# Performance work log

Hardware: AMD Instinct MI355X
Metric: run time of the kernel (lower is better)

Reference implementation:

```python
import jax, jax.numpy as jnp
import numpy as np


def _rconv(x, w, b):
    # reflection-pad 1 then 3x3 valid conv (same spatial size), NCHW/OIHW
    xp = jnp.pad(x, ((0, 0), (0, 0), (1, 1), (1, 1)), mode='reflect')
    y = jax.lax.conv_general_dilated(
        xp, w, window_strides=(1, 1), padding='VALID',
        dimension_numbers=('NCHW', 'OIHW', 'NCHW'))
    return y + b[None, :, None, None]


def setup_inputs() -> dict:
    key = jax.random.key(0)
    ks = jax.random.split(key, 12)
    B, C, H, W = 4, 256, 64, 64
    IC = 128  # inter_channels
    s = lambda fan_in: 1.0 / np.sqrt(fan_in)
    return {
        'query_feat': jax.random.normal(ks[0], (B, C, H, W), jnp.float32),
        'key_feat': jax.random.normal(ks[1], (B, C, H, W), jnp.float32),
        # 1x1 conv projections (stored as [out, in])
        'w_theta': jax.random.normal(ks[2], (IC, C), jnp.float32) * s(C),
        'b_theta': jnp.zeros((IC,), jnp.float32),
        'w_phi': jax.random.normal(ks[3], (IC, C), jnp.float32) * s(C),
        'b_phi': jnp.zeros((IC,), jnp.float32),
        # post-correlation block: conv(1->32), residual(32), conv(32->1)
        'w_in': jax.random.normal(ks[4], (32, 1, 3, 3), jnp.float32) * s(9),
        'b_in': jnp.zeros((32,), jnp.float32),
        'w_r1': jax.random.normal(ks[5], (32, 32, 3, 3), jnp.float32) * s(32 * 9),
        'b_r1': jnp.zeros((32,), jnp.float32),
        'w_r2': jax.random.normal(ks[6], (32, 32, 3, 3), jnp.float32) * s(32 * 9),
        'b_r2': jnp.zeros((32,), jnp.float32),
        'w_out': jax.random.normal(ks[7], (1, 32, 3, 3), jnp.float32) * s(32 * 9),
        'b_out': jnp.zeros((1,), jnp.float32),
    }


def reference(query_feat, key_feat, w_theta, b_theta, w_phi, b_phi,
              w_in, b_in, w_r1, b_r1, w_r2, b_r2, w_out, b_out):
    B, C, H, W = query_feat.shape
    N = H * W
    # 1x1 conv projections, flattened to sequences
    theta = jnp.einsum('oc,bchw->bohw', w_theta, query_feat) + b_theta[None, :, None, None]
    phi = jnp.einsum('oc,bchw->bohw', w_phi, key_feat) + b_phi[None, :, None, None]
    theta = theta.reshape(B, -1, N).transpose(0, 2, 1)  # [B, N, IC]
    phi = phi.reshape(B, -1, N)                          # [B, IC, N]
    # correlation matrix [B, N, N] then max over key positions
    f = jnp.matmul(theta, phi)
    sim = jnp.max(f, axis=-1).reshape(B, 1, H, W)
    # post-correlation conv refinement
    h = _rconv(sim, w_in, b_in)                      # 1 -> 32
    r = jax.nn.relu(_rconv(h, w_r1, b_r1))           # residual block
    r = _rconv(r, w_r2, b_r2)
    h = h + r
    out = _rconv(h, w_out, b_out)                    # 32 -> 1
    return out
```

## Files before the change

### kernel.cpp

```cpp
#include <hip/hip_runtime.h>

#define B_ 4
#define C_ 256
#define HH 64
#define WW 64
#define N_ 4096
#define IC_ 128
#define JC_ 8

typedef __attribute__((ext_vector_type(8))) short bf16x8;
typedef __attribute__((ext_vector_type(4))) float f32x4;

__device__ __forceinline__ short f2bf(float f) {
    unsigned u = __builtin_bit_cast(unsigned, f);
    unsigned r = (u + 0x7FFFu + ((u >> 16) & 1u)) >> 16;
    return (short)r;
}

__device__ __forceinline__ int refl(int v) {
    return v < 0 ? -v : (v > 63 ? 126 - v : v);
}

__global__ __launch_bounds__(256) void k_project(
    const float* __restrict__ qf, const float* __restrict__ kf,
    const float* __restrict__ wq, const float* __restrict__ wk,
    const float* __restrict__ bq, const float* __restrict__ bk,
    short* __restrict__ outq, short* __restrict__ outk) {
    int z = blockIdx.z;
    const float* x = z ? kf : qf;
    const float* wf = z ? wk : wq;
    const float* bias = z ? bk : bq;
    short* outT = z ? outk : outq;

    int b = blockIdx.y;
    int n0 = blockIdx.x * 64;
    int t = threadIdx.x;
    int lane = t & 63, wv = t >> 6;
    int l15 = lane & 15, q4 = lane >> 4;
    const float* xb = x + (size_t)b * C_ * N_;

    __shared__ float xs[2][32][68];

    f32x4 acc[8];
#pragma unroll
    for (int cf = 0; cf < 8; cf++) acc[cf] = (f32x4){0.f, 0.f, 0.f, 0.f};

    {
        int i0 = t, i1 = t + 256;
        int r0 = i0 >> 4, c0 = i0 & 15;
        int r1 = i1 >> 4, c1 = i1 & 15;
        *(f32x4*)(&xs[0][r0][c0 * 4]) = *(const f32x4*)(xb + (size_t)r0 * N_ + n0 + c0 * 4);
        *(f32x4*)(&xs[0][r1][c1 * 4]) = *(const f32x4*)(xb + (size_t)r1 * N_ + n0 + c1 * 4);
    }

    for (int ks = 0; ks < 8; ks++) {
        __syncthreads();
        int buf = ks & 1;
        if (ks < 7) {
            int cb = (ks + 1) * 32;
            int i0 = t, i1 = t + 256;
            int r0 = i0 >> 4, c0 = i0 & 15;
            int r1 = i1 >> 4, c1 = i1 & 15;
            *(f32x4*)(&xs[buf ^ 1][r0][c0 * 4]) =
                *(const f32x4*)(xb + (size_t)(cb + r0) * N_ + n0 + c0 * 4);
            *(f32x4*)(&xs[buf ^ 1][r1][c1 * 4]) =
                *(const f32x4*)(xb + (size_t)(cb + r1) * N_ + n0 + c1 * 4);
        }
        int cbase = ks * 32 + q4 * 8;
        bf16x8 a;
#pragma unroll
        for (int j = 0; j < 8; j++) a[j] = f2bf(xs[buf][q4 * 8 + j][wv * 16 + l15]);
#pragma unroll
        for (int cf = 0; cf < 8; cf++) {
            const float* wp = wf + (size_t)(cf * 16 + l15) * C_ + cbase;
            f32x4 wa = *(const f32x4*)wp;
            f32x4 wb = *(const f32x4*)(wp + 4);
            bf16x8 bfr;
            bfr[0] = f2bf(wa[0]); bfr[1] = f2bf(wa[1]);
            bfr[2] = f2bf(wa[2]); bfr[3] = f2bf(wa[3]);
            bfr[4] = f2bf(wb[0]); bfr[5] = f2bf(wb[1]);
            bfr[6] = f2bf(wb[2]); bfr[7] = f2bf(wb[3]);
            acc[cf] = __builtin_amdgcn_mfma_f32_16x16x32_bf16(a, bfr, acc[cf], 0, 0, 0);
        }
    }
#pragma unroll
    for (int cf = 0; cf < 8; cf++) {
        int ic = cf * 16 + l15;
        float bv = bias[ic];
#pragma unroll
        for (int r = 0; r < 4; r++) {
            int n = n0 + wv * 16 + q4 * 4 + r;
            outT[((size_t)b * N_ + n) * IC_ + ic] = f2bf(acc[cf][r] + bv);
        }
    }
}

__global__ __launch_bounds__(256, 4) void k_corr(const short* __restrict__ thetaT,
                                                 const short* __restrict__ phiT,
                                                 float* __restrict__ simp) {
    __shared__ short ph[2][64][136];

    int b = blockIdx.z, jc = blockIdx.y;
    int i0 = blockIdx.x * 128;
    int t = threadIdx.x;
    int lane = t & 63, w = t >> 6;
    int l15 = lane & 15, q4 = lane >> 4;

    const short* thb = thetaT + ((size_t)b * N_ + i0 + w * 32) * IC_;
    const short* phb = phiT + ((size_t)b * N_ + jc * (N_ / JC_)) * IC_;

    bf16x8 afr[2][4];
#pragma unroll
    for (int rf = 0; rf < 2; rf++)
#pragma unroll
        for (int ks = 0; ks < 4; ks++)
            afr[rf][ks] = *(const bf16x8*)(thb + (size_t)(rf * 16 + l15) * IC_ + ks * 32 + q4 * 8);

    int srow = t >> 4, sc8 = t & 15;
#pragma unroll
    for (int k = 0; k < 4; k++)
        *(bf16x8*)(&ph[0][srow + k * 16][sc8 * 8]) =
            *(const bf16x8*)(phb + (size_t)(srow + k * 16) * IC_ + sc8 * 8);

    f32x4 rmax[2];
#pragma unroll
    for (int rf = 0; rf < 2; rf++) rmax[rf] = (f32x4){-3.0e38f, -3.0e38f, -3.0e38f, -3.0e38f};

    const int NT = (N_ / JC_) / 64;
    for (int it = 0; it < NT; it++) {
        int buf = it & 1;
        __syncthreads();
        if (it < NT - 1) {
            int j0 = (it + 1) * 64;
#pragma unroll
            for (int k = 0; k < 4; k++)
                *(bf16x8*)(&ph[buf ^ 1][srow + k * 16][sc8 * 8]) =
                    *(const bf16x8*)(phb + (size_t)(j0 + srow + k * 16) * IC_ + sc8 * 8);
        }
#pragma unroll
        for (int jf = 0; jf < 4; jf++) {
            bf16x8 bfr[4];
#pragma unroll
            for (int ks = 0; ks < 4; ks++)
                bfr[ks] = *(const bf16x8*)(&ph[buf][jf * 16 + l15][ks * 32 + q4 * 8]);
#pragma unroll
            for (int rf = 0; rf < 2; rf++) {
                f32x4 a2 = (f32x4){0.f, 0.f, 0.f, 0.f};
#pragma unroll
                for (int ks = 0; ks < 4; ks++)
                    a2 = __builtin_amdgcn_mfma_f32_16x16x32_bf16(afr[rf][ks], bfr[ks], a2, 0, 0, 0);
#pragma unroll
                for (int r = 0; r < 4; r++) rmax[rf][r] = fmaxf(rmax[rf][r], a2[r]);
            }
        }
    }

#pragma unroll
    for (int rf = 0; rf < 2; rf++) {
#pragma unroll
        for (int r = 0; r < 4; r++) {
            float v = rmax[rf][r];
            v = fmaxf(v, __shfl_xor(v, 1));
            v = fmaxf(v, __shfl_xor(v, 2));
            v = fmaxf(v, __shfl_xor(v, 4));
            v = fmaxf(v, __shfl_xor(v, 8));
            rmax[rf][r] = v;
        }
    }
    if (l15 == 0) {
        float* sp = simp + ((size_t)(b * JC_ + jc)) * N_ + i0 + w * 32;
#pragma unroll
        for (int rf = 0; rf < 2; rf++)
#pragma unroll
            for (int r = 0; r < 4; r++) sp[rf * 16 + q4 * 4 + r] = rmax[rf][r];
    }
}

__global__ __launch_bounds__(256) void k_conv_in(const float* __restrict__ simp,
                                                 const float* __restrict__ w,
                                                 const float* __restrict__ bias,
                                                 float* __restrict__ h) {
    int y = blockIdx.x, b = blockIdx.y;
    int t = threadIdx.x;
    int oc = t >> 3, x8 = t & 7;
    __shared__ float srow[3][66];
    const float* sb = simp + (size_t)b * JC_ * N_;
    if (t < 192) {
        int r = t >> 6, x = t & 63;
        int idx = refl(y - 1 + r) * 64 + x;
        float v = -3.0e38f;
#pragma unroll
        for (int jc = 0; jc < JC_; jc++) v = fmaxf(v, sb[jc * N_ + idx]);
        srow[r][x + 1] = v;
    }
    if (t < 3) {
        int gy = refl(y - 1 + t);
        float vl = -3.0e38f, vr = -3.0e38f;
#pragma unroll
        for (int jc = 0; jc < JC_; jc++) {
            vl = fmaxf(vl, sb[jc * N_ + gy * 64 + 1]);
            vr = fmaxf(vr, sb[jc * N_ + gy * 64 + 62]);
        }
        srow[t][0] = vl;
        srow[t][65] = vr;
    }
    __syncthreads();

    float wr[9];
#pragma unroll
    for (int k = 0; k < 9; k++) wr[k] = w[oc * 9 + k];
    float bv = bias[oc];
    float acc[8];
#pragma unroll
    for (int xi = 0; xi < 8; xi++) acc[xi] = bv;
#pragma unroll
    for (int ky = 0; ky < 3; ky++)
#pragma unroll
        for (int kx = 0; kx < 3; kx++) {
            float wv2 = wr[ky * 3 + kx];
#pragma unroll
            for (int xi = 0; xi < 8; xi++) acc[xi] += wv2 * srow[ky][x8 * 8 + xi + kx];
        }
    float* op = h + (((size_t)b * 32 + oc) * 64 + y) * 64 + x8 * 8;
#pragma unroll
    for (int xi = 0; xi < 8; xi++) op[xi] = acc[xi];
}

template <bool RELU, bool ADD>
__global__ __launch_bounds__(256) void k_conv_r(const float* __restrict__ in,
                                                const float* __restrict__ w,
                                                const float* __restrict__ bias,
                                                float* __restrict__ out,
                                                const float* __restrict__ add) {
    int y = blockIdx.x, b = blockIdx.z;
    int oc0 = blockIdx.y * 16;
    int t = threadIdx.x;
    __shared__ float tile[32][3][68];
    __shared__ float wlds[32 * 16 * 12];

#pragma unroll
    for (int k = 0; k < 18; k++) {
        int id = t + k * 256;
        int ocl = id / 288;
        int rem = id - ocl * 288;
        int ic = rem / 9;
        int tap = rem - ic * 9;
        wlds[(ic * 16 + ocl) * 12 + tap] = w[(size_t)(oc0 + ocl) * 288 + rem];
    }

#pragma unroll
    for (int r = 0; r < 3; r++) {
        int gy = refl(y - 1 + r);
#pragma unroll
        for (int i = 0; i < 2; i++) {
            int idx = t + i * 256;
            int ic = idx >> 4, c4 = idx & 15;
            f32x4 v = *(const f32x4*)(in + (((size_t)b * 32 + ic) * 64 + gy) * 64 + c4 * 4);
#pragma unroll
            for (int s = 0; s < 4; s++) tile[ic][r][c4 * 4 + s + 1] = v[s];
        }
    }
    if (t < 96) {
        int ic = t / 3, r = t - ic * 3;
        int gy = refl(y - 1 + r);
        const float* row = in + (((size_t)b * 32 + ic) * 64 + gy) * 64;
        tile[ic][r][0] = row[1];
        tile[ic][r][65] = row[62];
    }
    __syncthreads();

    int ocl = t >> 4, x4 = (t & 15) * 4;
    float bv = bias[oc0 + ocl];
    float acc[4];
#pragma unroll
    for (int xi = 0; xi < 4; xi++) acc[xi] = bv;

#pragma unroll 2
    for (int ic = 0; ic < 32; ic++) {
        const float* wr = &wlds[(ic * 16 + ocl) * 12];
        f32x4 W0 = *(const f32x4*)(wr);
        f32x4 W1 = *(const f32x4*)(wr + 4);
        f32x4 W2 = *(const f32x4*)(wr + 8);
        float w0 = W0[0], w1 = W0[1], w2 = W0[2], w3 = W0[3];
        float w4 = W1[0], w5 = W1[1], w6 = W1[2], w7 = W1[3];
        float w8 = W2[0];
        float xr[3][8];
#pragma unroll
        for (int r = 0; r < 3; r++) {
            const float* rowp = &tile[ic][r][x4];
            f32x4 A = *(const f32x4*)(rowp);
            f32x4 Bv = *(const f32x4*)(rowp + 4);
            xr[r][0] = A[0]; xr[r][1] = A[1]; xr[r][2] = A[2]; xr[r][3] = A[3];
            xr[r][4] = Bv[0]; xr[r][5] = Bv[1]; xr[r][6] = Bv[2]; xr[r][7] = Bv[3];
        }
#pragma unroll
        for (int xi = 0; xi < 4; xi++) {
            acc[xi] += w0 * xr[0][xi] + w1 * xr[0][xi + 1] + w2 * xr[0][xi + 2] +
                       w3 * xr[1][xi] + w4 * xr[1][xi + 1] + w5 * xr[1][xi + 2] +
                       w6 * xr[2][xi] + w7 * xr[2][xi + 1] + w8 * xr[2][xi + 2];
        }
    }
    size_t off = (((size_t)b * 32 + oc0 + ocl) * 64 + y) * 64 + x4;
#pragma unroll
    for (int xi = 0; xi < 4; xi++) {
        float v = acc[xi];
        if (RELU) v = fmaxf(v, 0.f);
        if (ADD) v += add[off + xi];
        out[off + xi] = v;
    }
}

__global__ __launch_bounds__(256) void k_conv_out(const float* __restrict__ hb,
                                                  const float* __restrict__ w,
                                                  const float* __restrict__ bias,
                                                  float* __restrict__ outp) {
    int y = blockIdx.x, b = blockIdx.y;
    int t = threadIdx.x;
    int x = t & 63, g = t >> 6;
    __shared__ float red[4][64];
    __shared__ float wl[288];
    for (int k = t; k < 288; k += 256) wl[k] = w[k];
    __syncthreads();
    float acc = 0.f;
#pragma unroll
    for (int i = 0; i < 8; i++) {
        int ic = g * 8 + i;
        const float* wp = wl + ic * 9;
#pragma unroll
        for (int ky = 0; ky < 3; ky++) {
            int gy = refl(y + ky - 1);
            const float* row = hb + (((size_t)b * 32 + ic) * 64 + gy) * 64;
#pragma unroll
            for (int kx = 0; kx < 3; kx++) {
                int gx = refl(x + kx - 1);
                acc += wp[ky * 3 + kx] * row[gx];
            }
        }
    }
    red[g][x] = acc;
    __syncthreads();
    if (t < 64) {
        outp[((size_t)b * 64 + y) * 64 + x] =
            bias[0] + red[0][t] + red[1][t] + red[2][t] + red[3][t];
    }
}

extern "C" void kernel_launch(void* const* d_in, const int* in_sizes, int n_in,
                              void* d_out, int out_size, void* d_ws, size_t ws_size,
                              hipStream_t stream) {
    const float* q = (const float*)d_in[0];
    const float* kf = (const float*)d_in[1];
    const float* w_theta = (const float*)d_in[2];
    const float* b_theta = (const float*)d_in[3];
    const float* w_phi = (const float*)d_in[4];
    const float* b_phi = (const float*)d_in[5];
    const float* w_in = (const float*)d_in[6];
    const float* b_in = (const float*)d_in[7];
    const float* w_r1 = (const float*)d_in[8];
    const float* b_r1 = (const float*)d_in[9];
    const float* w_r2 = (const float*)d_in[10];
    const float* b_r2 = (const float*)d_in[11];
    const float* w_out = (const float*)d_in[12];
    const float* b_out = (const float*)d_in[13];
    float* out = (float*)d_out;

    char* ws = (char*)d_ws;
    short* thetaT = (short*)(ws);
    short* phiT = (short*)(ws + 4194304);
    float* simp = (float*)(ws + 8519680);
    float* h = (float*)(ws);
    float* r = (float*)(ws + 2097152);

    k_project<<<dim3(64, 4, 2), 256, 0, stream>>>(q, kf, w_theta, w_phi, b_theta, b_phi,
                                                  thetaT, phiT);
    k_corr<<<dim3(32, JC_, 4), 256, 0, stream>>>(thetaT, phiT, simp);
    k_conv_in<<<dim3(64, 4), 256, 0, stream>>>(simp, w_in, b_in, h);
    k_conv_r<true, false><<<dim3(64, 2, 4), 256, 0, stream>>>(h, w_r1, b_r1, r, nullptr);
    k_conv_r<false, true><<<dim3(64, 2, 4), 256, 0, stream>>>(r, w_r2, b_r2, h, h);
    k_conv_out<<<dim3(64, 4), 256, 0, stream>>>(h, w_out, b_out, out);
}
```

Measured before the change: 187.2 us.

## Pre-convert projection weights to bf16 and retile projection over output channels

Adds a small kernel that converts the theta/phi weight matrices to bf16 once per call, so the projection kernel loads bf16x8 fragments directly instead of loading fp32 and converting inside the inner loop. The projection tile shrinks from 64 to 32 spatial positions, which doubles the grid. Each wave now covers 32 output channels across two row fragments, so every weight fragment is reused for two MFMAs, where before each wave did all 128 channels for 16 positions. This cuts redundant weight conversion and global weight traffic per block, at the cost of one extra kernel launch and more blocks that each reload their own input tile.

```diff
diff --git a/kernel.cpp b/kernel.cpp
--- a/kernel.cpp
+++ b/kernel.cpp
@@ -21,76 +21,78 @@
     return v < 0 ? -v : (v > 63 ? 126 - v : v);
 }
 
+__global__ __launch_bounds__(256) void k_cvt_w(const float* __restrict__ wt,
+                                               const float* __restrict__ wp,
+                                               short* __restrict__ wtb,
+                                               short* __restrict__ wpb) {
+    int i = blockIdx.x * 256 + threadIdx.x;
+    wtb[i] = f2bf(wt[i]);
+    wpb[i] = f2bf(wp[i]);
+}
+
 __global__ __launch_bounds__(256) void k_project(
     const float* __restrict__ qf, const float* __restrict__ kf,
-    const float* __restrict__ wq, const float* __restrict__ wk,
+    const short* __restrict__ wq, const short* __restrict__ wk,
     const float* __restrict__ bq, const float* __restrict__ bk,
     short* __restrict__ outq, short* __restrict__ outk) {
     int z = blockIdx.z;
     const float* x = z ? kf : qf;
-    const float* wf = z ? wk : wq;
+    const short* wbf = z ? wk : wq;
     const float* bias = z ? bk : bq;
     short* outT = z ? outk : outq;
 
     int b = blockIdx.y;
-    int n0 = blockIdx.x * 64;
+    int n0 = blockIdx.x * 32;
     int t = threadIdx.x;
     int lane = t & 63, wv = t >> 6;
     int l15 = lane & 15, q4 = lane >> 4;
     const float* xb = x + (size_t)b * C_ * N_;
 
-    __shared__ float xs[2][32][68];
-
-    f32x4 acc[8];
-#pragma unroll
-    for (int cf = 0; cf < 8; cf++) acc[cf] = (f32x4){0.f, 0.f, 0.f, 0.f};
-
-    {
-        int i0 = t, i1 = t + 256;
-        int r0 = i0 >> 4, c0 = i0 & 15;
-        int r1 = i1 >> 4, c1 = i1 & 15;
-        *(f32x4*)(&xs[0][r0][c0 * 4]) = *(const f32x4*)(xb + (size_t)r0 * N_ + n0 + c0 * 4);
-        *(f32x4*)(&xs[0][r1][c1 * 4]) = *(const f32x4*)(xb + (size_t)r1 * N_ + n0 + c1 * 4);
-    }
+    __shared__ float xs[2][32][36];
+
+    f32x4 acc[2][2];
+#pragma unroll
+    for (int rf = 0; rf < 2; rf++)
+#pragma unroll
+        for (int cfi = 0; cfi < 2; cfi++) acc[rf][cfi] = (f32x4){0.f, 0.f, 0.f, 0.f};
+
+    int sr = t >> 3, sc = t & 7;
+    *(f32x4*)(&xs[0][sr][sc * 4]) = *(const f32x4*)(xb + (size_t)sr * N_ + n0 + sc * 4);
 
     for (int ks = 0; ks < 8; ks++) {
         __syncthreads();
         int buf = ks & 1;
         if (ks < 7) {
             int cb = (ks + 1) * 32;
-            int i0 = t, i1 = t + 256;
-            int r0 = i0 >> 4, c0 = i0 & 15;
-            int r1 = i1 >> 4, c1 = i1 & 15;
-            *(f32x4*)(&xs[buf ^ 1][r0][c0 * 4]) =
-                *(const f32x4*)(xb + (size_t)(cb + r0) * N_ + n0 + c0 * 4);
-            *(f32x4*)(&xs[buf ^ 1][r1][c1 * 4]) =
-                *(const f32x4*)(xb + (size_t)(cb + r1) * N_ + n0 + c1 * 4);
+            *(f32x4*)(&xs[buf ^ 1][sr][sc * 4]) =
+                *(const f32x4*)(xb + (size_t)(cb + sr) * N_ + n0 + sc * 4);
         }
         int cbase = ks * 32 + q4 * 8;
-        bf16x8 a;
-#pragma unroll
-        for (int j = 0; j < 8; j++) a[j] = f2bf(xs[buf][q4 * 8 + j][wv * 16 + l15]);
-#pragma unroll
-        for (int cf = 0; cf < 8; cf++) {
-            const float* wp = wf + (size_t)(cf * 16 + l15) * C_ + cbase;
-            f32x4 wa = *(const f32x4*)wp;
-            f32x4 wb = *(const f32x4*)(wp + 4);
-            bf16x8 bfr;
-            bfr[0] = f2bf(wa[0]); bfr[1] = f2bf(wa[1]);
-            bfr[2] = f2bf(wa[2]); bfr[3] = f2bf(wa[3]);
-            bfr[4] = f2bf(wb[0]); bfr[5] = f2bf(wb[1]);
-            bfr[6] = f2bf(wb[2]); bfr[7] = f2bf(wb[3]);
-            acc[cf] = __builtin_amdgcn_mfma_f32_16x16x32_bf16(a, bfr, acc[cf], 0, 0, 0);
-        }
-    }
-#pragma unroll
-    for (int cf = 0; cf < 8; cf++) {
-        int ic = cf * 16 + l15;
+        bf16x8 a[2];
+#pragma unroll
+        for (int rf = 0; rf < 2; rf++)
+#pragma unroll
+            for (int j = 0; j < 8; j++) a[rf][j] = f2bf(xs[buf][q4 * 8 + j][rf * 16 + l15]);
+#pragma unroll
+        for (int cfi = 0; cfi < 2; cfi++) {
+            int cf = wv * 2 + cfi;
+            bf16x8 bfr = *(const bf16x8*)(wbf + (size_t)(cf * 16 + l15) * C_ + cbase);
+#pragma unroll
+            for (int rf = 0; rf < 2; rf++)
+                acc[rf][cfi] = __builtin_amdgcn_mfma_f32_16x16x32_bf16(a[rf], bfr, acc[rf][cfi], 0, 0, 0);
+        }
+    }
+#pragma unroll
+    for (int cfi = 0; cfi < 2; cfi++) {
+        int ic = (wv * 2 + cfi) * 16 + l15;
         float bv = bias[ic];
 #pragma unroll
-        for (int r = 0; r < 4; r++) {
-            int n = n0 + wv * 16 + q4 * 4 + r;
-            outT[((size_t)b * N_ + n) * IC_ + ic] = f2bf(acc[cf][r] + bv);
+        for (int rf = 0; rf < 2; rf++) {
+#pragma unroll
+            for (int r = 0; r < 4; r++) {
+                int n = n0 + rf * 16 + q4 * 4 + r;
+                outT[((size_t)b * N_ + n) * IC_ + ic] = f2bf(acc[rf][cfi][r] + bv);
+            }
         }
     }
 }
@@ -367,12 +369,15 @@
     char* ws = (char*)d_ws;
     short* thetaT = (short*)(ws);
     short* phiT = (short*)(ws + 4194304);
+    short* wthb = (short*)(ws + 8388608);
+    short* wphb = (short*)(ws + 8454144);
     float* simp = (float*)(ws + 8519680);
     float* h = (float*)(ws);
     float* r = (float*)(ws + 2097152);
 
-    k_project<<<dim3(64, 4, 2), 256, 0, stream>>>(q, kf, w_theta, w_phi, b_theta, b_phi,
-                                                  thetaT, phiT);
+    k_cvt_w<<<128, 256, 0, stream>>>(w_theta, w_phi, wthb, wphb);
+    k_project<<<dim3(128, 4, 2), 256, 0, stream>>>(q, kf, wthb, wphb, b_theta, b_phi,
+                                                   thetaT, phiT);
     k_corr<<<dim3(32, JC_, 4), 256, 0, stream>>>(thetaT, phiT, simp);
     k_conv_in<<<dim3(64, 4), 256, 0, stream>>>(simp, w_in, b_in, h);
     k_conv_r<true, false><<<dim3(64, 2, 4), 256, 0, stream>>>(h, w_r1, b_r1, r, nullptr);
```

New measurement: 165.8 us, median of 2. 11.4% less time.
